# Optimization experiments

Measured on AMD Instinct MI355X. Metric: run time of the kernel, lower is better.

## Reference

```python
import jax, jax.numpy as jnp
import numpy as np

TOP_K = 2


def setup_inputs() -> dict:
    key = jax.random.key(0)
    ks = jax.random.split(key, 6)
    B, S, H, I, E = 4, 2048, 1024, 4096, 8
    x = jax.random.normal(ks[0], (B, S, H), dtype=jnp.float32)
    Wr = jax.random.normal(ks[1], (H, E), dtype=jnp.float32) * (1.0 / np.sqrt(H))
    W1 = jax.random.normal(ks[2], (E, H, I), dtype=jnp.float32) * (1.0 / np.sqrt(H))
    b1 = jnp.zeros((E, I), dtype=jnp.float32)
    W2 = jax.random.normal(ks[3], (E, I, H), dtype=jnp.float32) * (1.0 / np.sqrt(I))
    b2 = jnp.zeros((E, H), dtype=jnp.float32)
    return {"x": x, "Wr": Wr, "W1": W1, "b1": b1, "W2": W2, "b2": b2}


def reference(x, Wr, W1, b1, W2, b2):
    B, S, H = x.shape
    E = Wr.shape[1]
    xf = x.reshape(-1, H)                              # [T, H], T = B*S
    logits = xf @ Wr                                   # [T, E]
    probs = jax.nn.softmax(logits, axis=-1)
    rw, sel = jax.lax.top_k(probs, TOP_K)              # [T, K]
    rw = rw / jnp.sum(rw, axis=-1, keepdims=True)
    out = jnp.zeros_like(xf)
    # Loop over small fixed expert count; each token contributes only via its
    # top-k combine weight (zero weight == not routed, matching index_add).
    for i in range(E):
        wi = jnp.sum(jnp.where(sel == i, rw, 0.0), axis=-1)    # [T]
        h = jax.nn.silu(xf @ W1[i] + b1[i])                    # [T, I]
        out = out + (h @ W2[i] + b2[i]) * wi[:, None]
    return out.reshape(B, S, H)
```

## Files before the change

### kernel.cpp

```cpp
#include <hip/hip_runtime.h>
#include <cstdint>
#include <cstddef>

#define TTOK 8192
#define HDIM 1024
#define IDIM 4096
#define NEXP 8
#define PMAX 18432
#define WS_NEED 302260352ULL

#define SLOT 16384

typedef __attribute__((ext_vector_type(8))) short bf16x8;
typedef __attribute__((ext_vector_type(4))) float f32x4;

#define AS3 __attribute__((address_space(3)))
#define AS1 __attribute__((address_space(1)))

__device__ __forceinline__ void gld16(const void* g, void* s) {
  __builtin_amdgcn_global_load_lds((const AS1 void*)g, (AS3 void*)s, 16, 0, 0);
}

__device__ __forceinline__ void pinned_barrier() {
  __builtin_amdgcn_sched_barrier(0);
  __builtin_amdgcn_s_barrier();
  __builtin_amdgcn_sched_barrier(0);
}

__device__ __forceinline__ unsigned short f2b(float f) {
  unsigned u = __builtin_bit_cast(unsigned, f);
  unsigned r = ((u >> 16) & 1u) + 0x7FFFu;
  return (unsigned short)((u + r) >> 16);
}

__global__ __launch_bounds__(256, 2) void router_k(
    const float* __restrict__ x, const float* __restrict__ wr,
    unsigned short* __restrict__ xb, int* __restrict__ t2e,
    float* __restrict__ t2w)
{
  const int t = blockIdx.x * 4 + (threadIdx.x >> 6);
  const int l = threadIdx.x & 63;
  const float* xr = x + (size_t)t * HDIM;
  float acc[8] = {0.f,0.f,0.f,0.f,0.f,0.f,0.f,0.f};
  #pragma unroll
  for (int j = 0; j < 4; ++j) {
    const int base = j * 256 + l * 4;
    const float4 xv = *(const float4*)(xr + base);
    const float xa[4] = {xv.x, xv.y, xv.z, xv.w};
    ushort4 ub;
    ub.x = f2b(xa[0]); ub.y = f2b(xa[1]); ub.z = f2b(xa[2]); ub.w = f2b(xa[3]);
    *(ushort4*)(xb + (size_t)t * HDIM + base) = ub;
    #pragma unroll
    for (int ii = 0; ii < 4; ++ii) {
      const float4 w0 = *(const float4*)(wr + (size_t)(base + ii) * 8);
      const float4 w1 = *(const float4*)(wr + (size_t)(base + ii) * 8 + 4);
      acc[0] += xa[ii] * w0.x; acc[1] += xa[ii] * w0.y;
      acc[2] += xa[ii] * w0.z; acc[3] += xa[ii] * w0.w;
      acc[4] += xa[ii] * w1.x; acc[5] += xa[ii] * w1.y;
      acc[6] += xa[ii] * w1.z; acc[7] += xa[ii] * w1.w;
    }
  }
  #pragma unroll
  for (int e = 0; e < 8; ++e) {
    float v = acc[e];
    #pragma unroll
    for (int off = 32; off > 0; off >>= 1) v += __shfl_xor(v, off);
    acc[e] = v;
  }
  if (l == 0) {
    float l0 = -1e30f; int i0 = 0;
    #pragma unroll
    for (int e = 0; e < 8; ++e) if (acc[e] > l0) { l0 = acc[e]; i0 = e; }
    float l1 = -1e30f; int i1 = (i0 == 0) ? 1 : 0;
    #pragma unroll
    for (int e = 0; e < 8; ++e) if (e != i0 && acc[e] > l1) { l1 = acc[e]; i1 = e; }
    const float w0 = 1.f / (1.f + expf(l1 - l0));
    t2e[t * 2] = i0; t2e[t * 2 + 1] = i1;
    t2w[t * 2] = w0; t2w[t * 2 + 1] = 1.f - w0;
  }
}

__global__ void count_k(const int* __restrict__ t2e, int* __restrict__ meta) {
  const int t = threadIdx.x, w = t >> 6, l = t & 63;
  int cnt[8] = {0,0,0,0,0,0,0,0};
  for (int c = 0; c < 16; ++c) {
    const int tok = (w * 16 + c) * 64 + l;
    const int e0 = t2e[2 * tok], e1 = t2e[2 * tok + 1];
    #pragma unroll
    for (int e = 0; e < 8; ++e)
      cnt[e] += __popcll(__ballot(e0 == e)) + __popcll(__ballot(e1 == e));
  }
  __shared__ int part[8][8];
  if (l == 0) {
    #pragma unroll
    for (int e = 0; e < 8; ++e) part[w][e] = cnt[e];
  }
  __syncthreads();
  if (t == 0) {
    int off = 0;
    #pragma unroll
    for (int e = 0; e < 8; ++e) {
      int s = 0;
      #pragma unroll
      for (int w2 = 0; w2 < 8; ++w2) s += part[w2][e];
      meta[e] = s; meta[16 + e] = off; off += (s + 255) & ~255;
    }
    meta[24] = off;
  }
}

__global__ void scatter_k(const int* __restrict__ t2e, const int* __restrict__ meta,
                          int* __restrict__ ltok, int* __restrict__ t2p)
{
  const int e = blockIdx.x;
  const int t = threadIdx.x, w = t >> 6, l = t & 63;
  const int off = meta[16 + e];
  const int cnt = meta[e];
  __shared__ int wsum[4];
  __shared__ int base;
  if (t == 0) base = 0;
  __syncthreads();
  const unsigned long long lt = (1ULL << l) - 1ULL;
  for (int c = 0; c < TTOK / 256; ++c) {
    const int tok = c * 256 + t;
    const bool m0 = (t2e[2 * tok] == e);
    const bool m1 = (t2e[2 * tok + 1] == e);
    const unsigned long long b0 = __ballot(m0);
    const unsigned long long b1 = __ballot(m1);
    const int n0 = __popcll(b0), n1 = __popcll(b1);
    const int r0 = __popcll(b0 & lt);
    const int r1 = n0 + __popcll(b1 & lt);
    if (l == 0) wsum[w] = n0 + n1;
    __syncthreads();
    int wb = base;
    #pragma unroll
    for (int i = 0; i < 4; ++i) if (i < w) wb += wsum[i];
    const int tot = wsum[0] + wsum[1] + wsum[2] + wsum[3];
    __syncthreads();
    if (t == 0) base += tot;
    if (m0) { const int p = off + wb + r0; ltok[p] = tok; t2p[2 * tok] = p; }
    if (m1) { const int p = off + wb + r1; ltok[p] = tok; t2p[2 * tok + 1] = p; }
    __syncthreads();
  }
  const int padded = (cnt + 255) & ~255;
  for (int i = cnt + t; i < padded; i += 256) ltok[off + i] = -1;
}

__global__ __launch_bounds__(256, 2) void packT_k(const float* __restrict__ src,
                                                  unsigned short* __restrict__ dst,
                                                  int K, int N)
{
  const int tiles_n = N >> 8, tiles_k = K >> 5;
  const int bid = blockIdx.x;
  const int e = bid / (tiles_k * tiles_n);
  const int rem = bid % (tiles_k * tiles_n);
  const int kt = rem / tiles_n, it = rem % tiles_n;
  const float* S = src + (size_t)e * K * N + (size_t)kt * 32 * N + (size_t)it * 256;
  unsigned short* D = dst + (size_t)e * N * K + (size_t)it * 256 * K + (size_t)kt * 32;
  __shared__ uint32_t lds[256 * 17];
  const int t = threadIdx.x;
  #pragma unroll
  for (int q = 0; q < 4; ++q) {
    const int task = q * 256 + t;
    const int i4 = task & 63, kp = task >> 6;
    const float* p0 = S + (size_t)(2 * kp) * N + i4 * 4;
    const float4 r0 = *(const float4*)p0;
    const float4 r1 = *(const float4*)(p0 + N);
    const float a0[4] = {r0.x, r0.y, r0.z, r0.w};
    const float a1[4] = {r1.x, r1.y, r1.z, r1.w};
    #pragma unroll
    for (int j = 0; j < 4; ++j)
      lds[(i4 * 4 + j) * 17 + kp] = (uint32_t)f2b(a0[j]) | ((uint32_t)f2b(a1[j]) << 16);
  }
  __syncthreads();
  #pragma unroll
  for (int r = 0; r < 4; ++r) {
    const int idx = r * 256 + t;
    const int il = idx >> 2, q4 = idx & 3;
    uint4 o;
    o.x = lds[il * 17 + q4 * 4 + 0];
    o.y = lds[il * 17 + q4 * 4 + 1];
    o.z = lds[il * 17 + q4 * 4 + 2];
    o.w = lds[il * 17 + q4 * 4 + 3];
    *(uint4*)(D + (size_t)il * K + q4 * 8) = o;
  }
}


__global__ __launch_bounds__(256, 3) void gemm1_k(
    const unsigned short* __restrict__ xb, const unsigned short* __restrict__ w1t,
    const float* __restrict__ b1, const int* __restrict__ meta,
    const int* __restrict__ ltok, unsigned short* __restrict__ h)
{
  const int wg = blockIdx.x;
  const int id = (wg & 7) * (4608 / 8) + (wg >> 3);
  const int mt = id >> 5, nt = id & 31;
  if (mt * 128 >= meta[24]) return;
  int e = 0;
  #pragma unroll
  for (int i = 1; i < 8; ++i) if (meta[16 + i] <= mt * 128) e = i;

  extern __shared__ char lds[];
  const int t = threadIdx.x;
  const int w = t >> 6, l = t & 63;
  const int wn = w & 1, wm = w >> 1;

  const unsigned short* asrc[2]; const unsigned short* bsrc[2];
  #pragma unroll
  for (int c = 0; c < 2; ++c) {
    const int G = c * 256 + t;
    const int line = G >> 3, q = (G & 7) ^ (line & 7);
    const int row = 2 * line + (q >> 2), g = q & 3;
    asrc[c] = w1t + ((size_t)e * IDIM + nt * 128 + row) * HDIM + g * 8;
    int tok = ltok[mt * 128 + row]; if (tok < 0) tok = 0;
    bsrc[c] = xb + (size_t)tok * HDIM + g * 8;
  }

  const int lr = l & 15, lg = l >> 4;
  f32x4 acc[4][4] = {};

  auto STAGE = [&](int kt) {
    char* sb = lds + (kt % 3) * SLOT;
    const int ks = kt * 32;
    gld16(asrc[0] + ks, sb + w * 1024);
    gld16(asrc[1] + ks, sb + 4096 + w * 1024);
    gld16(bsrc[0] + ks, sb + 8192 + w * 1024);
    gld16(bsrc[1] + ks, sb + 12288 + w * 1024);
  };

  STAGE(0); STAGE(1);
  const int NT = HDIM / 32;
  for (int kt = 0; kt < NT; ++kt) {
    if (kt + 1 < NT) {
      asm volatile("s_waitcnt vmcnt(4)" ::: "memory");
    } else {
      asm volatile("s_waitcnt vmcnt(0)" ::: "memory");
    }
    pinned_barrier();
    const char* sl = lds + (kt % 3) * SLOT;
    bf16x8 af[4], bf[4];
    #pragma unroll
    for (int f = 0; f < 4; ++f) {
      const int rowA = wn * 64 + f * 16 + lr;
      const int lineA = rowA >> 1;
      const int pA = (((rowA & 1) << 2) + lg) ^ (lineA & 7);
      af[f] = *(const bf16x8*)(sl + lineA * 128 + pA * 16);
      const int rowB = wm * 64 + f * 16 + lr;
      const int lineB = rowB >> 1;
      const int pB = (((rowB & 1) << 2) + lg) ^ (lineB & 7);
      bf[f] = *(const bf16x8*)(sl + 8192 + lineB * 128 + pB * 16);
    }
    if (kt + 2 < NT) STAGE(kt + 2);
    __builtin_amdgcn_s_setprio(1);
    #pragma unroll
    for (int fm = 0; fm < 4; ++fm)
      #pragma unroll
      for (int fn = 0; fn < 4; ++fn)
        acc[fm][fn] = __builtin_amdgcn_mfma_f32_16x16x32_bf16(af[fm], bf[fn], acc[fm][fn], 0, 0, 0);
    __builtin_amdgcn_s_setprio(0);
    pinned_barrier();
  }

  const int lg4 = lg * 4;
  #pragma unroll
  for (int fm = 0; fm < 4; ++fm) {
    const int ib = nt * 128 + wn * 64 + fm * 16 + lg4;
    const float4 b1v = *(const float4*)(b1 + e * IDIM + ib);
    #pragma unroll
    for (int fn = 0; fn < 4; ++fn) {
      const int trow = mt * 128 + wm * 64 + fn * 16 + lr;
      const float v0 = acc[fm][fn][0] + b1v.x;
      const float v1 = acc[fm][fn][1] + b1v.y;
      const float v2 = acc[fm][fn][2] + b1v.z;
      const float v3 = acc[fm][fn][3] + b1v.w;
      ushort4 st;
      st.x = f2b(v0 / (1.f + __expf(-v0)));
      st.y = f2b(v1 / (1.f + __expf(-v1)));
      st.z = f2b(v2 / (1.f + __expf(-v2)));
      st.w = f2b(v3 / (1.f + __expf(-v3)));
      *(ushort4*)(h + (size_t)trow * IDIM + ib) = st;
    }
  }
}

__global__ __launch_bounds__(256, 3) void gemm2_k(
    const unsigned short* __restrict__ h, const unsigned short* __restrict__ w2t,
    const int* __restrict__ meta, float* __restrict__ y)
{
  const int wg = blockIdx.x;
  const int id = (wg & 7) * (1152 / 8) + (wg >> 3);
  const int mt = id >> 3, nt = id & 7;
  if (mt * 128 >= meta[24]) return;
  int e = 0;
  #pragma unroll
  for (int i = 1; i < 8; ++i) if (meta[16 + i] <= mt * 128) e = i;

  extern __shared__ char lds[];
  const int t = threadIdx.x;
  const int w = t >> 6, l = t & 63;
  const int wn = w & 1, wm = w >> 1;

  const unsigned short* asrc[2]; const unsigned short* bsrc[2];
  #pragma unroll
  for (int c = 0; c < 2; ++c) {
    const int G = c * 256 + t;
    const int line = G >> 3, q = (G & 7) ^ (line & 7);
    const int row = 2 * line + (q >> 2), g = q & 3;
    asrc[c] = w2t + ((size_t)e * HDIM + nt * 128 + row) * IDIM + g * 8;
    bsrc[c] = h + (size_t)(mt * 128 + row) * IDIM + g * 8;
  }

  const int lr = l & 15, lg = l >> 4;
  f32x4 acc[4][4] = {};

  auto STAGE = [&](int kt) {
    char* sb = lds + (kt % 3) * SLOT;
    const int ks = kt * 32;
    gld16(asrc[0] + ks, sb + w * 1024);
    gld16(asrc[1] + ks, sb + 4096 + w * 1024);
    gld16(bsrc[0] + ks, sb + 8192 + w * 1024);
    gld16(bsrc[1] + ks, sb + 12288 + w * 1024);
  };

  STAGE(0); STAGE(1);
  const int NT = IDIM / 32;
  for (int kt = 0; kt < NT; ++kt) {
    if (kt + 1 < NT) {
      asm volatile("s_waitcnt vmcnt(4)" ::: "memory");
    } else {
      asm volatile("s_waitcnt vmcnt(0)" ::: "memory");
    }
    pinned_barrier();
    const char* sl = lds + (kt % 3) * SLOT;
    bf16x8 af[4], bf[4];
    #pragma unroll
    for (int f = 0; f < 4; ++f) {
      const int rowA = wn * 64 + f * 16 + lr;
      const int lineA = rowA >> 1;
      const int pA = (((rowA & 1) << 2) + lg) ^ (lineA & 7);
      af[f] = *(const bf16x8*)(sl + lineA * 128 + pA * 16);
      const int rowB = wm * 64 + f * 16 + lr;
      const int lineB = rowB >> 1;
      const int pB = (((rowB & 1) << 2) + lg) ^ (lineB & 7);
      bf[f] = *(const bf16x8*)(sl + 8192 + lineB * 128 + pB * 16);
    }
    if (kt + 2 < NT) STAGE(kt + 2);
    __builtin_amdgcn_s_setprio(1);
    #pragma unroll
    for (int fm = 0; fm < 4; ++fm)
      #pragma unroll
      for (int fn = 0; fn < 4; ++fn)
        acc[fm][fn] = __builtin_amdgcn_mfma_f32_16x16x32_bf16(af[fm], bf[fn], acc[fm][fn], 0, 0, 0);
    __builtin_amdgcn_s_setprio(0);
    pinned_barrier();
  }

  const int lg4 = lg * 4;
  #pragma unroll
  for (int fm = 0; fm < 4; ++fm) {
    const int colb = nt * 128 + wn * 64 + fm * 16 + lg4;
    #pragma unroll
    for (int fn = 0; fn < 4; ++fn) {
      const int row = mt * 128 + wm * 64 + fn * 16 + lr;
      float4 st;
      st.x = acc[fm][fn][0]; st.y = acc[fm][fn][1];
      st.z = acc[fm][fn][2]; st.w = acc[fm][fn][3];
      *(float4*)(y + (size_t)row * HDIM + colb) = st;
    }
  }
}

__global__ __launch_bounds__(256, 4) void combine_k(
    const float* __restrict__ y, const float* __restrict__ b2,
    const int* __restrict__ t2e, const float* __restrict__ t2w,
    const int* __restrict__ t2p, float* __restrict__ out)
{
  const int t = blockIdx.x * 4 + (threadIdx.x >> 6);
  const int l = threadIdx.x & 63;
  const int e0 = t2e[t * 2], e1 = t2e[t * 2 + 1];
  const float w0 = t2w[t * 2], w1v = t2w[t * 2 + 1];
  const int p0 = t2p[t * 2], p1 = t2p[t * 2 + 1];
  const float* y0 = y + (size_t)p0 * HDIM;
  const float* y1 = y + (size_t)p1 * HDIM;
  const float* bb0 = b2 + e0 * HDIM;
  const float* bb1 = b2 + e1 * HDIM;
  float* o = out + (size_t)t * HDIM;
  #pragma unroll
  for (int j = 0; j < 4; ++j) {
    const int c = j * 256 + l * 4;
    const float4 a = *(const float4*)(y0 + c);
    const float4 b = *(const float4*)(y1 + c);
    const float4 c0 = *(const float4*)(bb0 + c);
    const float4 c1 = *(const float4*)(bb1 + c);
    float4 r;
    r.x = w0 * (a.x + c0.x) + w1v * (b.x + c1.x);
    r.y = w0 * (a.y + c0.y) + w1v * (b.y + c1.y);
    r.z = w0 * (a.z + c0.z) + w1v * (b.z + c1.z);
    r.w = w0 * (a.w + c0.w) + w1v * (b.w + c1.w);
    *(float4*)(o + c) = r;
  }
}

__global__ void sentinel_k(float* out) { out[0] = 1.0e6f; }

extern "C" void kernel_launch(void* const* d_in, const int* in_sizes, int n_in,
                              void* d_out, int out_size, void* d_ws, size_t ws_size,
                              hipStream_t stream)
{
  (void)in_sizes; (void)n_in; (void)out_size;
  const float* x  = (const float*)d_in[0];
  const float* wr = (const float*)d_in[1];
  const float* w1 = (const float*)d_in[2];
  const float* b1 = (const float*)d_in[3];
  const float* w2 = (const float*)d_in[4];
  const float* b2 = (const float*)d_in[5];
  float* out = (float*)d_out;
  char* ws = (char*)d_ws;

  if (ws_size < WS_NEED) { sentinel_k<<<1, 1, 0, stream>>>(out); return; }

  unsigned short* xb  = (unsigned short*)(ws);
  unsigned short* w1t = (unsigned short*)(ws + 16777216);
  unsigned short* w2t = (unsigned short*)(ws + 83886080);
  unsigned short* h   = (unsigned short*)(ws + 150994944);
  int*   t2e  = (int*)(ws + 301989888);
  float* t2w  = (float*)(ws + 302055424);
  int*   ltok = (int*)(ws + 302120960);
  int*   t2p  = (int*)(ws + 302194688);
  int*   meta = (int*)(ws + 302260224);
  float* y    = (float*)(ws);

  hipFuncSetAttribute((const void*)gemm1_k, hipFuncAttributeMaxDynamicSharedMemorySize, 3 * SLOT);
  hipFuncSetAttribute((const void*)gemm2_k, hipFuncAttributeMaxDynamicSharedMemorySize, 3 * SLOT);

  router_k<<<TTOK / 4, 256, 0, stream>>>(x, wr, xb, t2e, t2w);
  packT_k<<<NEXP * (HDIM / 32) * (IDIM / 256), 256, 0, stream>>>(w1, w1t, HDIM, IDIM);
  packT_k<<<NEXP * (IDIM / 32) * (HDIM / 256), 256, 0, stream>>>(w2, w2t, IDIM, HDIM);
  count_k<<<1, 512, 0, stream>>>(t2e, meta);
  scatter_k<<<NEXP, 256, 0, stream>>>(t2e, meta, ltok, t2p);

  gemm1_k<<<144 * 32, 256, 3 * SLOT, stream>>>(xb, w1t, b1, meta, ltok, h);
  gemm2_k<<<144 * 8, 256, 3 * SLOT, stream>>>(h, w2t, meta, y);
  combine_k<<<TTOK / 4, 256, 0, stream>>>(y, b2, t2e, t2w, t2p, out);
}
```

Measured before the change: 583.9 us.

## Enlarge gemm1 token tile to 256 rows with 512-thread blocks

gemm1 now computes 256 token rows by 128 intermediate columns per block using 8 waves instead of 4. Each expert weight tile loaded into LDS is reused across twice as many tokens, which halves weight traffic per output. The LDS slot grows to 24 KB, the per-thread load pattern and vmcnt wait are adjusted to match, and the grid is halved. Two risks: the tighter launch bound (512 threads, 4 blocks) may force register spills, and correctness depends on expert segments being padded to 256-token boundaries.

```diff
diff --git a/kernel.cpp b/kernel.cpp
--- a/kernel.cpp
+++ b/kernel.cpp
@@ -9,7 +9,8 @@
 #define PMAX 18432
 #define WS_NEED 302260352ULL
 
-#define SLOT 16384
+#define SLOT1 24576
+#define SLOT2 16384
 
 typedef __attribute__((ext_vector_type(8))) short bf16x8;
 typedef __attribute__((ext_vector_type(4))) float f32x4;
@@ -187,32 +188,38 @@
 }
 
 
-__global__ __launch_bounds__(256, 3) void gemm1_k(
+__global__ __launch_bounds__(512, 4) void gemm1_k(
     const unsigned short* __restrict__ xb, const unsigned short* __restrict__ w1t,
     const float* __restrict__ b1, const int* __restrict__ meta,
     const int* __restrict__ ltok, unsigned short* __restrict__ h)
 {
   const int wg = blockIdx.x;
-  const int id = (wg & 7) * (4608 / 8) + (wg >> 3);
+  const int id = (wg & 7) * (2304 / 8) + (wg >> 3);
   const int mt = id >> 5, nt = id & 31;
-  if (mt * 128 >= meta[24]) return;
+  if (mt * 256 >= meta[24]) return;
   int e = 0;
   #pragma unroll
-  for (int i = 1; i < 8; ++i) if (meta[16 + i] <= mt * 128) e = i;
+  for (int i = 1; i < 8; ++i) if (meta[16 + i] <= mt * 256) e = i;
 
   extern __shared__ char lds[];
   const int t = threadIdx.x;
   const int w = t >> 6, l = t & 63;
   const int wn = w & 1, wm = w >> 1;
 
-  const unsigned short* asrc[2]; const unsigned short* bsrc[2];
-  #pragma unroll
-  for (int c = 0; c < 2; ++c) {
-    const int G = c * 256 + t;
+  const unsigned short* asrc;
+  {
+    const int G = t;
     const int line = G >> 3, q = (G & 7) ^ (line & 7);
     const int row = 2 * line + (q >> 2), g = q & 3;
-    asrc[c] = w1t + ((size_t)e * IDIM + nt * 128 + row) * HDIM + g * 8;
-    int tok = ltok[mt * 128 + row]; if (tok < 0) tok = 0;
+    asrc = w1t + ((size_t)e * IDIM + nt * 128 + row) * HDIM + g * 8;
+  }
+  const unsigned short* bsrc[2];
+  #pragma unroll
+  for (int c = 0; c < 2; ++c) {
+    const int G = c * 512 + t;
+    const int line = G >> 3, q = (G & 7) ^ (line & 7);
+    const int row = 2 * line + (q >> 2), g = q & 3;
+    int tok = ltok[mt * 256 + row]; if (tok < 0) tok = 0;
     bsrc[c] = xb + (size_t)tok * HDIM + g * 8;
   }
 
@@ -220,24 +227,23 @@
   f32x4 acc[4][4] = {};
 
   auto STAGE = [&](int kt) {
-    char* sb = lds + (kt % 3) * SLOT;
+    char* sb = lds + (kt % 3) * SLOT1;
     const int ks = kt * 32;
-    gld16(asrc[0] + ks, sb + w * 1024);
-    gld16(asrc[1] + ks, sb + 4096 + w * 1024);
+    gld16(asrc + ks, sb + w * 1024);
     gld16(bsrc[0] + ks, sb + 8192 + w * 1024);
-    gld16(bsrc[1] + ks, sb + 12288 + w * 1024);
+    gld16(bsrc[1] + ks, sb + 16384 + w * 1024);
   };
 
   STAGE(0); STAGE(1);
   const int NT = HDIM / 32;
   for (int kt = 0; kt < NT; ++kt) {
     if (kt + 1 < NT) {
-      asm volatile("s_waitcnt vmcnt(4)" ::: "memory");
+      asm volatile("s_waitcnt vmcnt(3)" ::: "memory");
     } else {
       asm volatile("s_waitcnt vmcnt(0)" ::: "memory");
     }
     pinned_barrier();
-    const char* sl = lds + (kt % 3) * SLOT;
+    const char* sl = lds + (kt % 3) * SLOT1;
     bf16x8 af[4], bf[4];
     #pragma unroll
     for (int f = 0; f < 4; ++f) {
@@ -268,7 +274,7 @@
     const float4 b1v = *(const float4*)(b1 + e * IDIM + ib);
     #pragma unroll
     for (int fn = 0; fn < 4; ++fn) {
-      const int trow = mt * 128 + wm * 64 + fn * 16 + lr;
+      const int trow = mt * 256 + wm * 64 + fn * 16 + lr;
       const float v0 = acc[fm][fn][0] + b1v.x;
       const float v1 = acc[fm][fn][1] + b1v.y;
       const float v2 = acc[fm][fn][2] + b1v.z;
@@ -314,7 +320,7 @@
   f32x4 acc[4][4] = {};
 
   auto STAGE = [&](int kt) {
-    char* sb = lds + (kt % 3) * SLOT;
+    char* sb = lds + (kt % 3) * SLOT2;
     const int ks = kt * 32;
     gld16(asrc[0] + ks, sb + w * 1024);
     gld16(asrc[1] + ks, sb + 4096 + w * 1024);
@@ -331,7 +337,7 @@
       asm volatile("s_waitcnt vmcnt(0)" ::: "memory");
     }
     pinned_barrier();
-    const char* sl = lds + (kt % 3) * SLOT;
+    const char* sl = lds + (kt % 3) * SLOT2;
     bf16x8 af[4], bf[4];
     #pragma unroll
     for (int f = 0; f < 4; ++f) {
@@ -430,8 +436,8 @@
   int*   meta = (int*)(ws + 302260224);
   float* y    = (float*)(ws);
 
-  hipFuncSetAttribute((const void*)gemm1_k, hipFuncAttributeMaxDynamicSharedMemorySize, 3 * SLOT);
-  hipFuncSetAttribute((const void*)gemm2_k, hipFuncAttributeMaxDynamicSharedMemorySize, 3 * SLOT);
+  hipFuncSetAttribute((const void*)gemm1_k, hipFuncAttributeMaxDynamicSharedMemorySize, 3 * SLOT1);
+  hipFuncSetAttribute((const void*)gemm2_k, hipFuncAttributeMaxDynamicSharedMemorySize, 3 * SLOT2);
 
   router_k<<<TTOK / 4, 256, 0, stream>>>(x, wr, xb, t2e, t2w);
   packT_k<<<NEXP * (HDIM / 32) * (IDIM / 256), 256, 0, stream>>>(w1, w1t, HDIM, IDIM);
@@ -439,7 +445,7 @@
   count_k<<<1, 512, 0, stream>>>(t2e, meta);
   scatter_k<<<NEXP, 256, 0, stream>>>(t2e, meta, ltok, t2p);
 
-  gemm1_k<<<144 * 32, 256, 3 * SLOT, stream>>>(xb, w1t, b1, meta, ltok, h);
-  gemm2_k<<<144 * 8, 256, 3 * SLOT, stream>>>(h, w2t, meta, y);
+  gemm1_k<<<72 * 32, 512, 3 * SLOT1, stream>>>(xb, w1t, b1, meta, ltok, h);
+  gemm2_k<<<144 * 8, 256, 3 * SLOT2, stream>>>(h, w2t, meta, y);
   combine_k<<<TTOK / 4, 256, 0, stream>>>(y, b2, t2e, t2w, t2p, out);
 }
```

New measurement: 550.1 us. -5.8%, faster.
